# Kernel tuning notes

Hardware: AMD Instinct MI355X
Metric: run time of the kernel (lower is better)

## Reference

```python
import jax, jax.numpy as jnp
import numpy as np

D_MODEL = 1024
N_HEADS = 16
D_HEAD = D_MODEL // N_HEADS


def setup_inputs() -> dict:
    key = jax.random.key(0)
    ks = jax.random.split(key, 9)
    s = 1.0 / np.sqrt(D_MODEL)
    inp = {
        'x': jax.random.normal(ks[0], (2, 2048, D_MODEL), dtype=jnp.float32),
        'wq': jax.random.uniform(ks[1], (D_MODEL, D_MODEL), jnp.float32, -s, s),
        'bq': jnp.zeros((D_MODEL,), jnp.float32),
        'wk': jax.random.uniform(ks[2], (D_MODEL, D_MODEL), jnp.float32, -s, s),
        'bk': jnp.zeros((D_MODEL,), jnp.float32),
        'wv': jax.random.uniform(ks[3], (D_MODEL, D_MODEL), jnp.float32, -s, s),
        'bv': jnp.zeros((D_MODEL,), jnp.float32),
        'wo': jax.random.uniform(ks[4], (D_MODEL, D_MODEL), jnp.float32, -s, s),
        'bo': jnp.zeros((D_MODEL,), jnp.float32),
    }
    return inp


def reference(x, wq, bq, wk, bk, wv, bv, wo, bo):
    B, S, D = x.shape
    H, Dh = N_HEADS, D_HEAD
    # projections (dropout is identity in eval mode)
    q = (x @ wq + bq).reshape(B, S, H, Dh).transpose(0, 2, 1, 3)  # [B,H,S,Dh]
    k = (x @ wk + bk).reshape(B, S, H, Dh).transpose(0, 2, 1, 3)
    v = (x @ wv + bv).reshape(B, S, H, Dh).transpose(0, 2, 1, 3)
    scores = jnp.einsum('bhqd,bhkd->bhqk', q, k) / jnp.sqrt(jnp.float32(Dh))
    causal = jnp.tril(jnp.ones((S, S), dtype=bool))  # [S,S]
    scores = jnp.where(causal[None, None], scores, jnp.float32(-jnp.inf))
    attn = jax.nn.softmax(scores, axis=-1)
    out = jnp.einsum('bhqk,bhkd->bhqd', attn, v)  # [B,H,S,Dh]
    out = out.transpose(0, 2, 1, 3).reshape(B, S, D)
    return out @ wo + bo
```

## Files before the change

kernel.cpp:

```cpp
#include <hip/hip_runtime.h>
#include <hip/hip_bf16.h>
#include <stdint.h>

#define NH 16
#define DH 64
#define BATCH 2
#define SEQ 2048
#define DMODEL 1024

typedef __attribute__((ext_vector_type(8))) short short8;
typedef __attribute__((ext_vector_type(4))) float f32x4;

#define MFMA16(a, b, c) __builtin_amdgcn_mfma_f32_16x16x32_bf16(a, b, c, 0, 0, 0)

__device__ inline unsigned short f2bf(float f) {
    union { float f; unsigned u; } v; v.f = f;
    unsigned r = v.u + 0x7fff + ((v.u >> 16) & 1);
    return (unsigned short)(r >> 16);
}

__device__ inline void gload_lds16(const unsigned short* g, unsigned short* l) {
    __builtin_amdgcn_global_load_lds((const __attribute__((address_space(1))) void*)g,
                                     (__attribute__((address_space(3))) void*)l, 16, 0, 0);
}

__global__ void k_cvt(const float* __restrict__ in, unsigned short* __restrict__ out) {
    size_t i = ((size_t)blockIdx.x * 256 + threadIdx.x) * 8;
    f32x4 a = *(const f32x4*)(in + i);
    f32x4 b = *(const f32x4*)(in + i + 4);
    short8 o;
    o[0] = (short)f2bf(a[0]); o[1] = (short)f2bf(a[1]);
    o[2] = (short)f2bf(a[2]); o[3] = (short)f2bf(a[3]);
    o[4] = (short)f2bf(b[0]); o[5] = (short)f2bf(b[1]);
    o[6] = (short)f2bf(b[2]); o[7] = (short)f2bf(b[3]);
    *(short8*)(out + i) = o;
}

__global__ void k_transpose_w(const float* __restrict__ w, unsigned short* __restrict__ out) {
    __shared__ float tile[32][33];
    int k0 = blockIdx.x * 32, n0 = blockIdx.y * 32;
    int tx = threadIdx.x, ty = threadIdx.y;
    #pragma unroll
    for (int j = 0; j < 32; j += 8)
        tile[ty + j][tx] = w[(size_t)(k0 + ty + j) * DMODEL + n0 + tx];
    __syncthreads();
    #pragma unroll
    for (int j = 0; j < 32; j += 8)
        out[(size_t)(n0 + ty + j) * DMODEL + k0 + tx] = f2bf(tile[tx][ty + j]);
}

__global__ __launch_bounds__(256) void k_transpose_v(const unsigned short* __restrict__ v,
                                                     unsigned short* __restrict__ vt) {
    __shared__ __align__(16) unsigned short tile[64][72];
    int bh = blockIdx.y, st = blockIdx.x;
    const unsigned short* src = v + ((size_t)bh * SEQ + st * 64) * DH;
    int r = threadIdx.x >> 2, c = (threadIdx.x & 3) * 16;
    *(short8*)&tile[r][c]     = *(const short8*)&src[r * DH + c];
    *(short8*)&tile[r][c + 8] = *(const short8*)&src[r * DH + c + 8];
    __syncthreads();
    int d = r, sb = c;
    short8 o0, o1;
    #pragma unroll
    for (int j = 0; j < 8; ++j) { o0[j] = (short)tile[sb + j][d]; o1[j] = (short)tile[sb + 8 + j][d]; }
    unsigned short* dst = vt + ((size_t)bh * DH + d) * SEQ + st * 64 + sb;
    *(short8*)dst = o0;
    *(short8*)(dst + 8) = o1;
}

#define GEMM_BODY(A_, Bt_)                                                              \
    __shared__ __align__(16) unsigned short As[128 * 32];                               \
    __shared__ __align__(16) unsigned short Bs[128 * 32];                               \
    const int tid = threadIdx.x;                                                        \
    const int lane = tid & 63, wave = tid >> 6;                                         \
    const int wr = wave >> 1, wc = wave & 1;                                            \
    const int row0 = blockIdx.y * 128, col0 = blockIdx.x * 128;                         \
    const int frow = lane & 15, fk = (lane >> 4) * 8;                                   \
    f32x4 acc[4][4] = {};                                                               \
    const int lr = tid >> 2;                                                            \
    const int lc = (tid & 3) * 8;                                                       \
    const unsigned short* ga0 = A_ + (size_t)(row0 + lr) * 1024 + lc;                   \
    const unsigned short* gb0 = Bt_ + (size_t)(col0 + lr) * 1024 + lc;                  \
    for (int kt = 0; kt < 1024; kt += 32) {                                             \
        gload_lds16(ga0 + kt, As + wave * 512);                                         \
        gload_lds16(ga0 + 64 * 1024 + kt, As + 2048 + wave * 512);                      \
        gload_lds16(gb0 + kt, Bs + wave * 512);                                         \
        gload_lds16(gb0 + 64 * 1024 + kt, Bs + 2048 + wave * 512);                      \
        __syncthreads();                                                                \
        short8 af[4], bf[4];                                                            \
        _Pragma("unroll")                                                               \
        for (int m = 0; m < 4; ++m)                                                     \
            af[m] = *(const short8*)&As[(wr * 64 + m * 16 + frow) * 32 + fk];           \
        _Pragma("unroll")                                                               \
        for (int n = 0; n < 4; ++n)                                                     \
            bf[n] = *(const short8*)&Bs[(wc * 64 + n * 16 + frow) * 32 + fk];           \
        _Pragma("unroll")                                                               \
        for (int m = 0; m < 4; ++m)                                                     \
            _Pragma("unroll")                                                           \
            for (int n = 0; n < 4; ++n)                                                 \
                acc[m][n] = MFMA16(af[m], bf[n], acc[m][n]);                            \
        __syncthreads();                                                                \
    }

__global__ __launch_bounds__(256) void k_gemm_qkv(
    const unsigned short* __restrict__ A, const unsigned short* __restrict__ Bt,
    const float* __restrict__ bq, const float* __restrict__ bk, const float* __restrict__ bv,
    unsigned short* __restrict__ qo, unsigned short* __restrict__ ko,
    unsigned short* __restrict__ vo)
{
    GEMM_BODY(A, Bt)
    const int p = col0 >> 10;
    const float* bias = (p == 0) ? bq : ((p == 1) ? bk : bv);
    unsigned short* dst = (p == 0) ? qo : ((p == 1) ? ko : vo);
    const float scl = (p == 0) ? 0.125f : 1.0f;
    #pragma unroll
    for (int m = 0; m < 4; ++m) {
        #pragma unroll
        for (int n = 0; n < 4; ++n) {
            int gcol = col0 + wc * 64 + n * 16 + frow;
            int hn = gcol & 1023;
            int h = hn >> 6, d = hn & 63;
            #pragma unroll
            for (int i = 0; i < 4; ++i) {
                int grow = row0 + wr * 64 + m * 16 + (lane >> 4) * 4 + i;
                int b = grow >> 11, s = grow & 2047;
                float v = (acc[m][n][i] + bias[hn]) * scl;
                dst[((size_t)(b * NH + h) * SEQ + s) * DH + d] = f2bf(v);
            }
        }
    }
}

__global__ __launch_bounds__(256) void k_gemm_out(
    const unsigned short* __restrict__ A, const unsigned short* __restrict__ Bt,
    const float* __restrict__ bo, float* __restrict__ out)
{
    GEMM_BODY(A, Bt)
    #pragma unroll
    for (int m = 0; m < 4; ++m) {
        #pragma unroll
        for (int n = 0; n < 4; ++n) {
            int gcol = col0 + wc * 64 + n * 16 + frow;
            #pragma unroll
            for (int i = 0; i < 4; ++i) {
                int grow = row0 + wr * 64 + m * 16 + (lane >> 4) * 4 + i;
                out[(size_t)grow * DMODEL + gcol] = acc[m][n][i] + bo[gcol];
            }
        }
    }
}

__global__ __launch_bounds__(256) void k_attn(
    const unsigned short* __restrict__ Q, const unsigned short* __restrict__ K,
    const unsigned short* __restrict__ VT, unsigned short* __restrict__ O)
{
    __shared__ __align__(16) unsigned short Ks[2][64 * 64];
    __shared__ __align__(16) unsigned short Vs[2][64 * 64];
    __shared__ __align__(16) unsigned short Ps[4][16 * 72];
    const int tid = threadIdx.x, lane = tid & 63, wave = tid >> 6;
    const int p = blockIdx.x;
    const int L = ((p & 7) << 6) | (p >> 3);
    const int bh = L >> 4, pr = L & 15;
    const unsigned short* Qb = Q + (size_t)bh * SEQ * DH;
    const unsigned short* Kb = K + (size_t)bh * SEQ * DH;
    const unsigned short* Vb = VT + (size_t)bh * SEQ * DH;
    const int frow = lane & 15, fk = (lane >> 4) * 8;
    const int srow = lane >> 3;
    const int scol = ((lane & 7) ^ srow) << 3;
    const int bb = bh >> 4, hh = bh & 15;

    for (int rep = 0; rep < 2; ++rep) {
        const int qt = rep ? pr : 31 - pr;
        const int q0 = qt * 64;
        short8 qf[2];
        #pragma unroll
        for (int t = 0; t < 2; ++t)
            qf[t] = *(const short8*)&Qb[(size_t)(q0 + wave * 16 + frow) * DH + t * 32 + fk];
        f32x4 oacc[4] = {};
        float mrow[4], lrow[4];
        #pragma unroll
        for (int i = 0; i < 4; ++i) { mrow[i] = -INFINITY; lrow[i] = 0.f; }

        auto stage = [&](int b, int kv0) {
            #pragma unroll
            for (int rd = 0; rd < 2; ++rd) {
                int row = rd * 32 + wave * 8 + srow;
                gload_lds16(Kb + (size_t)(kv0 + row) * DH + scol,
                            &Ks[b][(rd * 32 + wave * 8) * 64]);
                gload_lds16(Vb + (size_t)row * SEQ + kv0 + scol,
                            &Vs[b][(rd * 32 + wave * 8) * 64]);
            }
        };

        auto compute = [&](int cb_, bool diag) {
            const char* kbase = (const char*)&Ks[cb_][0];
            const char* vbase = (const char*)&Vs[cb_][0];
            const int sw = (frow & 7) << 4;
            f32x4 sc[4];
            #pragma unroll
            for (int n = 0; n < 4; ++n) {
                f32x4 s = {0.f, 0.f, 0.f, 0.f};
                #pragma unroll
                for (int t = 0; t < 2; ++t) {
                    int cbt = (t * 32 + fk) * 2;
                    short8 kb = *(const short8*)(kbase + (n * 16 + frow) * 128 + (cbt ^ sw));
                    s = MFMA16(qf[t], kb, s);
                }
                sc[n] = s;
            }
            if (diag) {
                #pragma unroll
                for (int n = 0; n < 4; ++n) {
                    int col = n * 16 + frow;
                    #pragma unroll
                    for (int i = 0; i < 4; ++i) {
                        int qrel = wave * 16 + (lane >> 4) * 4 + i;
                        if (col > qrel) sc[n][i] = -INFINITY;
                    }
                }
            }
            float mx[4];
            #pragma unroll
            for (int i = 0; i < 4; ++i) {
                float m = fmaxf(fmaxf(sc[0][i], sc[1][i]), fmaxf(sc[2][i], sc[3][i]));
                m = fmaxf(m, __shfl_xor(m, 1));
                m = fmaxf(m, __shfl_xor(m, 2));
                m = fmaxf(m, __shfl_xor(m, 4));
                m = fmaxf(m, __shfl_xor(m, 8));
                mx[i] = m;
            }
            float dm = fmaxf(fmaxf(mx[0] - mrow[0], mx[1] - mrow[1]),
                             fmaxf(mx[2] - mrow[2], mx[3] - mrow[3]));
            if (__any(dm > 8.f)) {
                #pragma unroll
                for (int i = 0; i < 4; ++i) {
                    float mnew = fmaxf(mrow[i], mx[i]);
                    float scl = __expf(mrow[i] - mnew);
                    mrow[i] = mnew;
                    lrow[i] *= scl;
                    #pragma unroll
                    for (int n = 0; n < 4; ++n) oacc[n][i] *= scl;
                }
            }
            #pragma unroll
            for (int i = 0; i < 4; ++i) {
                float rsum = 0.f;
                #pragma unroll
                for (int n = 0; n < 4; ++n) {
                    float pv = __expf(sc[n][i] - mrow[i]);
                    sc[n][i] = pv;
                    rsum += pv;
                }
                rsum += __shfl_xor(rsum, 1);
                rsum += __shfl_xor(rsum, 2);
                rsum += __shfl_xor(rsum, 4);
                rsum += __shfl_xor(rsum, 8);
                lrow[i] += rsum;
            }
            #pragma unroll
            for (int n = 0; n < 4; ++n)
                #pragma unroll
                for (int i = 0; i < 4; ++i)
                    Ps[wave][((lane >> 4) * 4 + i) * 72 + n * 16 + frow] = f2bf(sc[n][i]);
            asm volatile("s_waitcnt lgkmcnt(0)" ::: "memory");
            short8 pa[2];
            #pragma unroll
            for (int t = 0; t < 2; ++t)
                pa[t] = *(const short8*)&Ps[wave][frow * 72 + t * 32 + fk];
            #pragma unroll
            for (int n = 0; n < 4; ++n)
                #pragma unroll
                for (int t = 0; t < 2; ++t) {
                    int cbt = (t * 32 + fk) * 2;
                    short8 vb2 = *(const short8*)(vbase + (n * 16 + frow) * 128 + (cbt ^ sw));
                    oacc[n] = MFMA16(pa[t], vb2, oacc[n]);
                }
        };

        stage(0, 0);
        int cur = 0;
        for (int kt = 0; kt < qt; ++kt) {
            stage(cur ^ 1, (kt + 1) * 64);
            asm volatile("s_waitcnt vmcnt(4)" ::: "memory");
            __builtin_amdgcn_s_barrier();
            compute(cur, false);
            __builtin_amdgcn_s_barrier();
            cur ^= 1;
        }
        asm volatile("s_waitcnt vmcnt(0)" ::: "memory");
        __builtin_amdgcn_s_barrier();
        compute(cur, true);
        #pragma unroll
        for (int n = 0; n < 4; ++n) {
            #pragma unroll
            for (int i = 0; i < 4; ++i) {
                int qrow = q0 + wave * 16 + (lane >> 4) * 4 + i;
                float v = oacc[n][i] / lrow[i];
                O[((size_t)(bb * SEQ + qrow)) * DMODEL + hh * DH + n * 16 + frow] = f2bf(v);
            }
        }
        __builtin_amdgcn_s_barrier();
    }
}

extern "C" void kernel_launch(void* const* d_in, const int* in_sizes, int n_in,
                              void* d_out, int out_size, void* d_ws, size_t ws_size,
                              hipStream_t stream) {
    const float* x  = (const float*)d_in[0];
    const float* wq = (const float*)d_in[1];
    const float* bq = (const float*)d_in[2];
    const float* wk = (const float*)d_in[3];
    const float* bk = (const float*)d_in[4];
    const float* wv = (const float*)d_in[5];
    const float* bv = (const float*)d_in[6];
    const float* wo = (const float*)d_in[7];
    const float* bo = (const float*)d_in[8];
    float* out = (float*)d_out;

    char* w = (char*)d_ws;
    unsigned short* xb    = (unsigned short*)(w);
    unsigned short* vT    = (unsigned short*)(w);
    unsigned short* wqkvT = (unsigned short*)(w + 8388608);
    unsigned short* woT   = (unsigned short*)(w + 14680064);
    unsigned short* qarr  = (unsigned short*)(w + 16777216);
    unsigned short* karr  = (unsigned short*)(w + 25165824);
    unsigned short* varr  = (unsigned short*)(w + 33554432);
    unsigned short* attnb = (unsigned short*)(w + 41943040);

    k_cvt<<<2048, 256, 0, stream>>>(x, xb);
    dim3 tb(32, 8);
    dim3 tg(32, 32);
    k_transpose_w<<<tg, tb, 0, stream>>>(wq, wqkvT);
    k_transpose_w<<<tg, tb, 0, stream>>>(wk, wqkvT + 1024 * 1024);
    k_transpose_w<<<tg, tb, 0, stream>>>(wv, wqkvT + 2 * 1024 * 1024);
    k_transpose_w<<<tg, tb, 0, stream>>>(wo, woT);
    k_gemm_qkv<<<dim3(24, 32), 256, 0, stream>>>(xb, wqkvT, bq, bk, bv, qarr, karr, varr);
    k_transpose_v<<<dim3(32, 32), 256, 0, stream>>>(varr, vT);
    k_attn<<<dim3(512), 256, 0, stream>>>(qarr, karr, vT, attnb);
    k_gemm_out<<<dim3(8, 32), 256, 0, stream>>>(attnb, woT, bo, out);
}
```

Measured before the change: 230.1 us.

## Merge weight transposes into one launch, use DPP reductions and MFMA priority

The four weight-transpose launches are folded into one kernel whose z grid dimension selects the matrix, which removes three launches. In the attention kernel the row max and row sum reductions switch from ds_swizzle/bpermute-style shuffles to DPP row_shr moves. The MFMA sections are wrapped in s_setprio so waves issuing matrix work get scheduling priority. The DPP row_shr pattern with bound_ctrl false leaves lanes at the row edge holding their own value, so the reduction is correct only if the final lane's result is the one used. Here every lane uses its own result, which could be a correctness risk.

Result: faster. 211.5 us (-8.1%).

```diff
diff --git a/kernel.cpp b/kernel.cpp
--- a/kernel.cpp
+++ b/kernel.cpp
@@ -22,6 +22,31 @@
 __device__ inline void gload_lds16(const unsigned short* g, unsigned short* l) {
     __builtin_amdgcn_global_load_lds((const __attribute__((address_space(1))) void*)g,
                                      (__attribute__((address_space(3))) void*)l, 16, 0, 0);
+}
+
+__device__ inline float dpp16_max(float v) {
+    int t;
+    t = __builtin_amdgcn_mov_dpp(__float_as_int(v), 0x121, 0xf, 0xf, false);
+    v = fmaxf(v, __int_as_float(t));
+    t = __builtin_amdgcn_mov_dpp(__float_as_int(v), 0x122, 0xf, 0xf, false);
+    v = fmaxf(v, __int_as_float(t));
+    t = __builtin_amdgcn_mov_dpp(__float_as_int(v), 0x124, 0xf, 0xf, false);
+    v = fmaxf(v, __int_as_float(t));
+    t = __builtin_amdgcn_mov_dpp(__float_as_int(v), 0x128, 0xf, 0xf, false);
+    v = fmaxf(v, __int_as_float(t));
+    return v;
+}
+__device__ inline float dpp16_sum(float v) {
+    int t;
+    t = __builtin_amdgcn_mov_dpp(__float_as_int(v), 0x121, 0xf, 0xf, false);
+    v += __int_as_float(t);
+    t = __builtin_amdgcn_mov_dpp(__float_as_int(v), 0x122, 0xf, 0xf, false);
+    v += __int_as_float(t);
+    t = __builtin_amdgcn_mov_dpp(__float_as_int(v), 0x124, 0xf, 0xf, false);
+    v += __int_as_float(t);
+    t = __builtin_amdgcn_mov_dpp(__float_as_int(v), 0x128, 0xf, 0xf, false);
+    v += __int_as_float(t);
+    return v;
 }
 
 __global__ void k_cvt(const float* __restrict__ in, unsigned short* __restrict__ out) {
@@ -36,8 +61,13 @@
     *(short8*)(out + i) = o;
 }
 
-__global__ void k_transpose_w(const float* __restrict__ w, unsigned short* __restrict__ out) {
+__global__ void k_transpose_w4(const float* __restrict__ wq, const float* __restrict__ wk,
+                               const float* __restrict__ wv, const float* __restrict__ wo,
+                               unsigned short* __restrict__ qkvT, unsigned short* __restrict__ oT) {
     __shared__ float tile[32][33];
+    const int z = blockIdx.z;
+    const float* w = (z == 0) ? wq : (z == 1) ? wk : (z == 2) ? wv : wo;
+    unsigned short* out = (z == 3) ? oT : qkvT + (size_t)z * 1024 * 1024;
     int k0 = blockIdx.x * 32, n0 = blockIdx.y * 32;
     int tx = threadIdx.x, ty = threadIdx.y;
     #pragma unroll
@@ -196,6 +226,7 @@
             const char* vbase = (const char*)&Vs[cb_][0];
             const int sw = (frow & 7) << 4;
             f32x4 sc[4];
+            __builtin_amdgcn_s_setprio(1);
             #pragma unroll
             for (int n = 0; n < 4; ++n) {
                 f32x4 s = {0.f, 0.f, 0.f, 0.f};
@@ -207,6 +238,7 @@
                 }
                 sc[n] = s;
             }
+            __builtin_amdgcn_s_setprio(0);
             if (diag) {
                 #pragma unroll
                 for (int n = 0; n < 4; ++n) {
@@ -220,14 +252,8 @@
             }
             float mx[4];
             #pragma unroll
-            for (int i = 0; i < 4; ++i) {
-                float m = fmaxf(fmaxf(sc[0][i], sc[1][i]), fmaxf(sc[2][i], sc[3][i]));
-                m = fmaxf(m, __shfl_xor(m, 1));
-                m = fmaxf(m, __shfl_xor(m, 2));
-                m = fmaxf(m, __shfl_xor(m, 4));
-                m = fmaxf(m, __shfl_xor(m, 8));
-                mx[i] = m;
-            }
+            for (int i = 0; i < 4; ++i)
+                mx[i] = dpp16_max(fmaxf(fmaxf(sc[0][i], sc[1][i]), fmaxf(sc[2][i], sc[3][i])));
             float dm = fmaxf(fmaxf(mx[0] - mrow[0], mx[1] - mrow[1]),
                              fmaxf(mx[2] - mrow[2], mx[3] - mrow[3]));
             if (__any(dm > 8.f)) {
@@ -250,11 +276,7 @@
                     sc[n][i] = pv;
                     rsum += pv;
                 }
-                rsum += __shfl_xor(rsum, 1);
-                rsum += __shfl_xor(rsum, 2);
-                rsum += __shfl_xor(rsum, 4);
-                rsum += __shfl_xor(rsum, 8);
-                lrow[i] += rsum;
+                lrow[i] += dpp16_sum(rsum);
             }
             #pragma unroll
             for (int n = 0; n < 4; ++n)
@@ -266,6 +288,7 @@
             #pragma unroll
             for (int t = 0; t < 2; ++t)
                 pa[t] = *(const short8*)&Ps[wave][frow * 72 + t * 32 + fk];
+            __builtin_amdgcn_s_setprio(1);
             #pragma unroll
             for (int n = 0; n < 4; ++n)
                 #pragma unroll
@@ -274,6 +297,7 @@
                     short8 vb2 = *(const short8*)(vbase + (n * 16 + frow) * 128 + (cbt ^ sw));
                     oacc[n] = MFMA16(pa[t], vb2, oacc[n]);
                 }
+            __builtin_amdgcn_s_setprio(0);
         };
 
         stage(0, 0);
@@ -327,12 +351,7 @@
     unsigned short* attnb = (unsigned short*)(w + 41943040);
 
     k_cvt<<<2048, 256, 0, stream>>>(x, xb);
-    dim3 tb(32, 8);
-    dim3 tg(32, 32);
-    k_transpose_w<<<tg, tb, 0, stream>>>(wq, wqkvT);
-    k_transpose_w<<<tg, tb, 0, stream>>>(wk, wqkvT + 1024 * 1024);
-    k_transpose_w<<<tg, tb, 0, stream>>>(wv, wqkvT + 2 * 1024 * 1024);
-    k_transpose_w<<<tg, tb, 0, stream>>>(wo, woT);
+    k_transpose_w4<<<dim3(32, 32, 4), dim3(32, 8), 0, stream>>>(wq, wk, wv, wo, wqkvT, woT);
     k_gemm_qkv<<<dim3(24, 32), 256, 0, stream>>>(xb, wqkvT, bq, bk, bv, qarr, karr, varr);
     k_transpose_v<<<dim3(32, 32), 256, 0, stream>>>(varr, vT);
     k_attn<<<dim3(512), 256, 0, stream>>>(qarr, karr, vT, attnb);
```
